# Performance work log

Hardware: AMD Instinct MI355X
Metric: run time of the kernel (lower is better)

## Reference

```python
import jax, jax.numpy as jnp
import numpy as np

N = 50000      # nodes
E = 800000     # edges
D_IN = 300     # input node feature dim
D_H = 96       # hidden dim
D_OUT = 2      # classes
G = 64         # graphs in batch


def setup_inputs() -> dict:
    key = jax.random.key(0)
    ks = jax.random.split(key, 10)
    x = jax.random.normal(ks[0], (N, D_IN), dtype=jnp.float32)
    src = jax.random.randint(ks[1], (E,), 0, N, dtype=jnp.int32)
    dst = jax.random.randint(ks[2], (E,), 0, N, dtype=jnp.int32)
    batch = jnp.sort(jax.random.randint(ks[3], (N,), 0, G, dtype=jnp.int32))
    # GCNConv: linear weight (no bias in lin), separate additive bias (PyG default)
    W1 = jax.random.normal(ks[4], (D_IN, D_H), jnp.float32) / np.sqrt(D_IN)
    b1 = jnp.zeros((D_H,), jnp.float32)
    W2 = jax.random.normal(ks[5], (D_H, D_H), jnp.float32) / np.sqrt(D_H)
    b2 = jnp.zeros((D_H,), jnp.float32)
    Wfc = jax.random.normal(ks[6], (D_H, D_OUT), jnp.float32) / np.sqrt(D_H)
    bfc = jnp.zeros((D_OUT,), jnp.float32)
    return {"x": x, "W1": W1, "b1": b1, "W2": W2, "b2": b2,
            "Wfc": Wfc, "bfc": bfc, "src": src, "dst": dst, "batch": batch}


def _gcn_conv(h_in, W, b, src, dst, deg_inv_sqrt):
    """PyG GCNConv with self-loops: out = D^-1/2 (A+I) D^-1/2 (h W) + b."""
    h = h_in @ W                                   # [N, F] transform first
    norm = deg_inv_sqrt[src] * deg_inv_sqrt[dst]   # [E]
    msg = h[src] * norm[:, None]                   # gather + scale (dominant traffic)
    agg = jax.ops.segment_sum(msg, dst, num_segments=N)
    agg = agg + h * (deg_inv_sqrt * deg_inv_sqrt)[:, None]  # self-loop term
    return agg + b


def reference(x, W1, b1, W2, b2, Wfc, bfc, src, dst, batch):
    # degree with self loops, computed on destination nodes (PyG convention)
    deg = jax.ops.segment_sum(jnp.ones((E,), x.dtype), dst, num_segments=N) + 1.0
    dis = jax.lax.rsqrt(deg)
    h = jax.nn.relu(_gcn_conv(x, W1, b1, src, dst, dis))   # dropout = identity (eval)
    h = jax.nn.relu(_gcn_conv(h, W2, b2, src, dst, dis))
    # global mean pool over per-graph node segments
    counts = jax.ops.segment_sum(jnp.ones((N,), x.dtype), batch, num_segments=G)
    pooled = jax.ops.segment_sum(h, batch, num_segments=G) / jnp.maximum(counts, 1.0)[:, None]
    return pooled @ Wfc + bfc                               # [G, D_OUT]
```

## Files before the change

kernel.cpp:

```cpp
#include <hip/hip_runtime.h>
#include <hip/hip_bf16.h>

#define NN 50000
#define NE 800000
#define DIN 300
#define KP1 320
#define DH 96
#define DOUTC 2
#define NG 64

#define NKB 10
#define NFRAG (NKB * 6 * 64)

#define DSTRIDE 64

typedef __attribute__((ext_vector_type(8))) short bf16x8;
typedef __attribute__((ext_vector_type(4))) float f32x4;

__device__ inline unsigned short f2bf(float f) {
    unsigned int u = __float_as_uint(f);
    unsigned int r = (u + 0x7fffu + ((u >> 16) & 1u)) >> 16;
    return (unsigned short)r;
}
__device__ inline float b2f(unsigned short u) {
    return __uint_as_float((unsigned int)u << 16);
}

__global__ void k_init(int* cnt, float* pooled, int* gcnt) {
    int i = blockIdx.x * blockDim.x + threadIdx.x;
    if (i < NN) cnt[i] = 0;
    if (i < NG * DH) pooled[i] = 0.f;
    if (i < NG) gcnt[i] = 0;
}

__global__ void k_scatcnt(const int* __restrict__ src, const int* __restrict__ dst,
                          int* cnt, unsigned short* __restrict__ esrc) {
    int e = blockIdx.x * blockDim.x + threadIdx.x;
    if (e < NE) {
        int d = dst[e];
        int pos = atomicAdd(&cnt[d], 1);
        if (pos < DSTRIDE) esrc[(size_t)d * DSTRIDE + pos] = (unsigned short)src[e];
    }
}

__global__ void k_dis(const int* __restrict__ cnt, float* __restrict__ dis) {
    int i = blockIdx.x * blockDim.x + threadIdx.x;
    if (i < NN) dis[i] = rsqrtf(1.0f + (float)cnt[i]);
}

__global__ void k_wt(const float* __restrict__ W, unsigned short* __restrict__ WT,
                     int K, int KPAD) {
    int i = blockIdx.x * blockDim.x + threadIdx.x;
    if (i >= DH * KPAD) return;
    int j = i / KPAD, k = i - j * KPAD;
    WT[i] = (k < K) ? f2bf(W[(size_t)k * DH + j]) : (unsigned short)0;
}

__global__ void k_wt1f(const float* __restrict__ W, unsigned short* __restrict__ WF) {
    int g = blockIdx.x * blockDim.x + threadIdx.x;
    if (g >= NFRAG * 8) return;
    int j = g & 7;
    int f = g >> 3;
    int lane = f & 63;
    int ft = f >> 6;
    int t = ft % 6;
    int i = ft / 6;
    int row = (lane & 15) + 16 * t;
    int col = i * 32 + (lane >> 4) * 8 + j;
    WF[g] = (col < DIN) ? f2bf(W[(size_t)col * DH + row]) : (unsigned short)0;
}

__global__ __launch_bounds__(256) void k_gemm1(const float* __restrict__ A,
        const unsigned short* __restrict__ WF, unsigned short* __restrict__ Cb) {
    __shared__ unsigned short ldsB[NFRAG * 8];
    const int tid = threadIdx.x;
    {
        const uint4* srcv = (const uint4*)WF;
        uint4* dstv = (uint4*)ldsB;
        #pragma unroll
        for (int f = 0; f < NFRAG / 256; ++f)
            dstv[f * 256 + tid] = srcv[f * 256 + tid];
    }
    __syncthreads();

    const int wv = tid >> 6;
    const int lane = tid & 63;
    const int m = lane & 15;
    const int quad = lane >> 4;
    const int row = blockIdx.x * 64 + wv * 16 + m;
    const int arow = row < NN ? row : NN - 1;
    const float* ap = A + (size_t)arow * DIN + quad * 8;
    const float4 z4 = make_float4(0.f, 0.f, 0.f, 0.f);
    const bf16x8* lb = (const bf16x8*)ldsB;
    f32x4 acc[6];
    #pragma unroll
    for (int t = 0; t < 6; ++t) acc[t] = (f32x4){0.f, 0.f, 0.f, 0.f};

    float4 pa[4][2];
    #pragma unroll
    for (int i = 0; i < 3; ++i) {
        int kb = i * 32 + quad * 8;
        pa[i][0] = (kb + 4 <= DIN) ? *(const float4*)(ap + i * 32) : z4;
        pa[i][1] = (kb + 8 <= DIN) ? *(const float4*)(ap + i * 32 + 4) : z4;
    }

    #pragma unroll
    for (int i = 0; i < NKB; ++i) {
        if (i + 3 < NKB) {
            int kb = (i + 3) * 32 + quad * 8;
            pa[(i + 3) & 3][0] = (kb + 4 <= DIN) ? *(const float4*)(ap + (i + 3) * 32) : z4;
            pa[(i + 3) & 3][1] = (kb + 8 <= DIN) ? *(const float4*)(ap + (i + 3) * 32 + 4) : z4;
        }
        float4 a0 = pa[i & 3][0], a1 = pa[i & 3][1];
        bf16x8 af;
        af[0] = (short)f2bf(a0.x); af[1] = (short)f2bf(a0.y);
        af[2] = (short)f2bf(a0.z); af[3] = (short)f2bf(a0.w);
        af[4] = (short)f2bf(a1.x); af[5] = (short)f2bf(a1.y);
        af[6] = (short)f2bf(a1.z); af[7] = (short)f2bf(a1.w);
        #pragma unroll
        for (int t = 0; t < 6; ++t) {
            bf16x8 bf = lb[(i * 6 + t) * 64 + lane];
            acc[t] = __builtin_amdgcn_mfma_f32_16x16x32_bf16(af, bf, acc[t], 0, 0, 0);
        }
    }
    const int rbase = blockIdx.x * 64 + wv * 16 + quad * 4;
    #pragma unroll
    for (int r = 0; r < 4; ++r) {
        int rr = rbase + r;
        if (rr < NN) {
            unsigned short* cp = Cb + (size_t)rr * DH + m;
            #pragma unroll
            for (int t = 0; t < 6; ++t) cp[t * 16] = f2bf(acc[t][r]);
        }
    }
}

__global__ __launch_bounds__(256) void k_gemm2(const unsigned short* __restrict__ Ab,
        const unsigned short* __restrict__ WT, unsigned short* __restrict__ Cb) {
    const int tid = threadIdx.x;
    const int wv = tid >> 6;
    const int lane = tid & 63;
    const int m = lane & 15;
    const int quad = lane >> 4;
    const int row = blockIdx.x * 64 + wv * 16 + m;
    const int arow = row < NN ? row : NN - 1;
    const unsigned short* ap = Ab + (size_t)arow * DH + quad * 8;
    const unsigned short* wp = WT + (size_t)m * DH + quad * 8;
    bf16x8 af[3], bf[3][6];
    #pragma unroll
    for (int i = 0; i < 3; ++i) af[i] = *(const bf16x8*)(ap + i * 32);
    #pragma unroll
    for (int i = 0; i < 3; ++i)
        #pragma unroll
        for (int t = 0; t < 6; ++t)
            bf[i][t] = *(const bf16x8*)(wp + (size_t)t * 16 * DH + i * 32);
    f32x4 acc[6];
    #pragma unroll
    for (int t = 0; t < 6; ++t) acc[t] = (f32x4){0.f, 0.f, 0.f, 0.f};
    #pragma unroll
    for (int i = 0; i < 3; ++i)
        #pragma unroll
        for (int t = 0; t < 6; ++t)
            acc[t] = __builtin_amdgcn_mfma_f32_16x16x32_bf16(af[i], bf[i][t], acc[t], 0, 0, 0);
    const int rbase = blockIdx.x * 64 + wv * 16 + quad * 4;
    #pragma unroll
    for (int r = 0; r < 4; ++r) {
        int rr = rbase + r;
        if (rr < NN) {
            unsigned short* cp = Cb + (size_t)rr * DH + m;
            #pragma unroll
            for (int t = 0; t < 6; ++t) cp[t * 16] = f2bf(acc[t][r]);
        }
    }
}

#define QH (DH / 4)
template <bool BFOUT>
__global__ void k_agg(const ushort4* __restrict__ hb, const float* __restrict__ dis,
                      const int* __restrict__ cnt,
                      const unsigned short* __restrict__ esrc,
                      const float4* __restrict__ bias4, float4* __restrict__ fout,
                      ushort4* __restrict__ bout) {
    int gid = blockIdx.x * blockDim.x + threadIdx.x;
    if (gid >= NN * QH) return;
    int n = gid / QH;
    int q = gid - n * QH;
    int count = cnt[n];
    if (count > DSTRIDE) count = DSTRIDE;
    const int beg = n * DSTRIDE;
    const int end = beg + count;
    float dn = dis[n];
    ushort4 u0 = hb[(size_t)n * QH + q];
    float4 acc = make_float4(dn * b2f(u0.x), dn * b2f(u0.y), dn * b2f(u0.z), dn * b2f(u0.w));
    int e = beg;
    for (; e + 3 < end; e += 4) {
        int s0 = esrc[e], s1 = esrc[e + 1], s2 = esrc[e + 2], s3 = esrc[e + 3];
        float d0 = dis[s0], d1 = dis[s1], d2 = dis[s2], d3 = dis[s3];
        ushort4 v0 = hb[(size_t)s0 * QH + q];
        ushort4 v1 = hb[(size_t)s1 * QH + q];
        ushort4 v2 = hb[(size_t)s2 * QH + q];
        ushort4 v3 = hb[(size_t)s3 * QH + q];
        acc.x = fmaf(d0, b2f(v0.x), acc.x); acc.y = fmaf(d0, b2f(v0.y), acc.y);
        acc.z = fmaf(d0, b2f(v0.z), acc.z); acc.w = fmaf(d0, b2f(v0.w), acc.w);
        acc.x = fmaf(d1, b2f(v1.x), acc.x); acc.y = fmaf(d1, b2f(v1.y), acc.y);
        acc.z = fmaf(d1, b2f(v1.z), acc.z); acc.w = fmaf(d1, b2f(v1.w), acc.w);
        acc.x = fmaf(d2, b2f(v2.x), acc.x); acc.y = fmaf(d2, b2f(v2.y), acc.y);
        acc.z = fmaf(d2, b2f(v2.z), acc.z); acc.w = fmaf(d2, b2f(v2.w), acc.w);
        acc.x = fmaf(d3, b2f(v3.x), acc.x); acc.y = fmaf(d3, b2f(v3.y), acc.y);
        acc.z = fmaf(d3, b2f(v3.z), acc.z); acc.w = fmaf(d3, b2f(v3.w), acc.w);
    }
    for (; e < end; ++e) {
        int s = esrc[e];
        float ds = dis[s];
        ushort4 v = hb[(size_t)s * QH + q];
        acc.x = fmaf(ds, b2f(v.x), acc.x);
        acc.y = fmaf(ds, b2f(v.y), acc.y);
        acc.z = fmaf(ds, b2f(v.z), acc.z);
        acc.w = fmaf(ds, b2f(v.w), acc.w);
    }
    float4 b = bias4[q];
    float4 r;
    r.x = fmaxf(fmaf(dn, acc.x, b.x), 0.f);
    r.y = fmaxf(fmaf(dn, acc.y, b.y), 0.f);
    r.z = fmaxf(fmaf(dn, acc.z, b.z), 0.f);
    r.w = fmaxf(fmaf(dn, acc.w, b.w), 0.f);
    if (BFOUT) {
        ushort4 o;
        o.x = f2bf(r.x); o.y = f2bf(r.y); o.z = f2bf(r.z); o.w = f2bf(r.w);
        bout[gid] = o;
    } else {
        fout[gid] = r;
    }
}

#define PNODES 32
__global__ void k_pool_partial(const float* __restrict__ h, const int* __restrict__ batch,
                               float* __restrict__ pooled, int* __restrict__ gcnt) {
    __shared__ int sbatch[PNODES];
    const int n0 = blockIdx.x * PNODES;
    const int nend = min(n0 + PNODES, NN);
    const int cnt = nend - n0;
    const int f = threadIdx.x;
    if (f < cnt) sbatch[f] = batch[n0 + f];
    __syncthreads();
    if (f < DH) {
        float acc = 0.f;
        int cur = sbatch[0];
        for (int i = 0; i < cnt; ++i) {
            int g = sbatch[i];
            if (g != cur) {
                atomicAdd(&pooled[cur * DH + f], acc);
                acc = 0.f; cur = g;
            }
            acc += h[(size_t)(n0 + i) * DH + f];
        }
        atomicAdd(&pooled[cur * DH + f], acc);
    } else if (f == DH) {
        int c = 0;
        int cur = sbatch[0];
        for (int i = 0; i < cnt; ++i) {
            int g = sbatch[i];
            if (g != cur) { atomicAdd(&gcnt[cur], c); c = 0; cur = g; }
            ++c;
        }
        atomicAdd(&gcnt[cur], c);
    }
}

__global__ void k_fc(const float* __restrict__ pooled, const int* __restrict__ gcnt,
                     const float* __restrict__ Wfc, const float* __restrict__ bfc,
                     float* __restrict__ out) {
    const int t = threadIdx.x;
    if (t >= NG * DOUTC) return;
    const int g = t / DOUTC;
    const int c = t - g * DOUTC;
    float inv = 1.f / fmaxf((float)gcnt[g], 1.f);
    float acc = bfc[c];
    #pragma unroll 8
    for (int j = 0; j < DH; ++j)
        acc += pooled[g * DH + j] * inv * Wfc[j * DOUTC + c];
    out[g * DOUTC + c] = acc;
}

extern "C" void kernel_launch(void* const* d_in, const int* in_sizes, int n_in,
                              void* d_out, int out_size, void* d_ws, size_t ws_size,
                              hipStream_t stream) {
    const float* x   = (const float*)d_in[0];
    const float* W1  = (const float*)d_in[1];
    const float* b1  = (const float*)d_in[2];
    const float* W2  = (const float*)d_in[3];
    const float* b2  = (const float*)d_in[4];
    const float* Wfc = (const float*)d_in[5];
    const float* bfc = (const float*)d_in[6];
    const int* src   = (const int*)d_in[7];
    const int* dst   = (const int*)d_in[8];
    const int* batch = (const int*)d_in[9];
    float* out = (float*)d_out;

    unsigned short* hb  = (unsigned short*)d_ws;
    unsigned short* a1b = hb + (size_t)NN * DH;
    float* hbuf  = (float*)(a1b + (size_t)NN * DH);
    float* dis   = hbuf + (size_t)NN * DH;
    float* pooled= dis + NN;
    int* cnt     = (int*)(pooled + NG * DH);
    int* gcnt    = cnt + NN;
    unsigned short* esrc = (unsigned short*)(gcnt + NG);
    unsigned short* wt1f = esrc + (size_t)NN * DSTRIDE;
    unsigned short* wt2  = wt1f + NFRAG * 8;

    const int TB = 256;
    k_init<<<(NN + TB - 1) / TB, TB, 0, stream>>>(cnt, pooled, gcnt);
    k_scatcnt<<<(NE + TB - 1) / TB, TB, 0, stream>>>(src, dst, cnt, esrc);
    k_dis<<<(NN + TB - 1) / TB, TB, 0, stream>>>(cnt, dis);
    k_wt1f<<<(NFRAG * 8 + TB - 1) / TB, TB, 0, stream>>>(W1, wt1f);
    k_wt<<<(DH * DH + TB - 1) / TB, TB, 0, stream>>>(W2, wt2, DH, DH);

    k_gemm1<<<(NN + 63) / 64, 256, 0, stream>>>(x, wt1f, hb);
    k_agg<true><<<(NN * QH + TB - 1) / TB, TB, 0, stream>>>(
        (const ushort4*)hb, dis, cnt, esrc, (const float4*)b1,
        nullptr, (ushort4*)a1b);
    k_gemm2<<<(NN + 63) / 64, 256, 0, stream>>>(a1b, wt2, hb);
    k_agg<false><<<(NN * QH + TB - 1) / TB, TB, 0, stream>>>(
        (const ushort4*)hb, dis, cnt, esrc, (const float4*)b2,
        (float4*)hbuf, nullptr);
    k_pool_partial<<<(NN + PNODES - 1) / PNODES, 128, 0, stream>>>(hbuf, batch, pooled, gcnt);
    k_fc<<<1, 128, 0, stream>>>(pooled, gcnt, Wfc, bfc, out);
}
```

Before: 262.0 us.

## Fuse edge scatter into GEMM1, pooling into second aggregation, merge prep kernels

Merges init and weight-layout kernels into one prep kernel and moves the edge-bucketing scatter into the tail of the first GEMM kernel. The second aggregation now atomically accumulates its ReLU output directly into per-graph pooled sums, removing the fp32 hidden buffer and the separate pooling kernel. Graph node counts are recovered by binary search over the sorted batch array in the final FC kernel. This cuts launches and a large write/read, but adds heavily contended float atomics on a small pooled array.

```diff
diff --git a/kernel.cpp b/kernel.cpp
--- a/kernel.cpp
+++ b/kernel.cpp
@@ -13,6 +13,8 @@
 #define NFRAG (NKB * 6 * 64)
 
 #define DSTRIDE 64
+#define NB1 ((NN + 63) / 64)
+#define EPB 1024
 
 typedef __attribute__((ext_vector_type(8))) short bf16x8;
 typedef __attribute__((ext_vector_type(4))) float f32x4;
@@ -26,20 +28,26 @@
     return __uint_as_float((unsigned int)u << 16);
 }
 
-__global__ void k_init(int* cnt, float* pooled, int* gcnt) {
+__global__ void k_prep(int* cnt, float* pooled,
+                       const float* __restrict__ W1, unsigned short* __restrict__ wt1f,
+                       const float* __restrict__ W2, unsigned short* __restrict__ wt2) {
     int i = blockIdx.x * blockDim.x + threadIdx.x;
     if (i < NN) cnt[i] = 0;
     if (i < NG * DH) pooled[i] = 0.f;
-    if (i < NG) gcnt[i] = 0;
-}
-
-__global__ void k_scatcnt(const int* __restrict__ src, const int* __restrict__ dst,
-                          int* cnt, unsigned short* __restrict__ esrc) {
-    int e = blockIdx.x * blockDim.x + threadIdx.x;
-    if (e < NE) {
-        int d = dst[e];
-        int pos = atomicAdd(&cnt[d], 1);
-        if (pos < DSTRIDE) esrc[(size_t)d * DSTRIDE + pos] = (unsigned short)src[e];
+    if (i < NFRAG * 8) {
+        int j = i & 7;
+        int f = i >> 3;
+        int lane = f & 63;
+        int ft = f >> 6;
+        int t = ft % 6;
+        int kb = ft / 6;
+        int row = (lane & 15) + 16 * t;
+        int col = kb * 32 + (lane >> 4) * 8 + j;
+        wt1f[i] = (col < DIN) ? f2bf(W1[(size_t)col * DH + row]) : (unsigned short)0;
+    }
+    if (i < DH * DH) {
+        int j = i / DH, k = i - j * DH;
+        wt2[i] = f2bf(W2[(size_t)k * DH + j]);
     }
 }
 
@@ -48,30 +56,10 @@
     if (i < NN) dis[i] = rsqrtf(1.0f + (float)cnt[i]);
 }
 
-__global__ void k_wt(const float* __restrict__ W, unsigned short* __restrict__ WT,
-                     int K, int KPAD) {
-    int i = blockIdx.x * blockDim.x + threadIdx.x;
-    if (i >= DH * KPAD) return;
-    int j = i / KPAD, k = i - j * KPAD;
-    WT[i] = (k < K) ? f2bf(W[(size_t)k * DH + j]) : (unsigned short)0;
-}
-
-__global__ void k_wt1f(const float* __restrict__ W, unsigned short* __restrict__ WF) {
-    int g = blockIdx.x * blockDim.x + threadIdx.x;
-    if (g >= NFRAG * 8) return;
-    int j = g & 7;
-    int f = g >> 3;
-    int lane = f & 63;
-    int ft = f >> 6;
-    int t = ft % 6;
-    int i = ft / 6;
-    int row = (lane & 15) + 16 * t;
-    int col = i * 32 + (lane >> 4) * 8 + j;
-    WF[g] = (col < DIN) ? f2bf(W[(size_t)col * DH + row]) : (unsigned short)0;
-}
-
-__global__ __launch_bounds__(256) void k_gemm1(const float* __restrict__ A,
-        const unsigned short* __restrict__ WF, unsigned short* __restrict__ Cb) {
+__global__ __launch_bounds__(256) void k_gemm1s(const float* __restrict__ A,
+        const unsigned short* __restrict__ WF, unsigned short* __restrict__ Cb,
+        const int* __restrict__ src, const int* __restrict__ dst,
+        int* cnt, unsigned short* __restrict__ esrc) {
     __shared__ unsigned short ldsB[NFRAG * 8];
     const int tid = threadIdx.x;
     {
@@ -131,6 +119,17 @@
             unsigned short* cp = Cb + (size_t)rr * DH + m;
             #pragma unroll
             for (int t = 0; t < 6; ++t) cp[t * 16] = f2bf(acc[t][r]);
+        }
+    }
+
+    const int ebase = blockIdx.x * EPB;
+    #pragma unroll
+    for (int k = 0; k < EPB / 256; ++k) {
+        int e = ebase + k * 256 + tid;
+        if (e < NE) {
+            int d = dst[e];
+            int pos = atomicAdd(&cnt[d], 1);
+            if (pos < DSTRIDE) esrc[(size_t)d * DSTRIDE + pos] = (unsigned short)src[e];
         }
     }
 }
@@ -179,7 +178,8 @@
 __global__ void k_agg(const ushort4* __restrict__ hb, const float* __restrict__ dis,
                       const int* __restrict__ cnt,
                       const unsigned short* __restrict__ esrc,
-                      const float4* __restrict__ bias4, float4* __restrict__ fout,
+                      const float4* __restrict__ bias4,
+                      const int* __restrict__ batch, float* __restrict__ pooled,
                       ushort4* __restrict__ bout) {
     int gid = blockIdx.x * blockDim.x + threadIdx.x;
     if (gid >= NN * QH) return;
@@ -229,52 +229,27 @@
         o.x = f2bf(r.x); o.y = f2bf(r.y); o.z = f2bf(r.z); o.w = f2bf(r.w);
         bout[gid] = o;
     } else {
-        fout[gid] = r;
-    }
-}
-
-#define PNODES 32
-__global__ void k_pool_partial(const float* __restrict__ h, const int* __restrict__ batch,
-                               float* __restrict__ pooled, int* __restrict__ gcnt) {
-    __shared__ int sbatch[PNODES];
-    const int n0 = blockIdx.x * PNODES;
-    const int nend = min(n0 + PNODES, NN);
-    const int cnt = nend - n0;
-    const int f = threadIdx.x;
-    if (f < cnt) sbatch[f] = batch[n0 + f];
-    __syncthreads();
-    if (f < DH) {
-        float acc = 0.f;
-        int cur = sbatch[0];
-        for (int i = 0; i < cnt; ++i) {
-            int g = sbatch[i];
-            if (g != cur) {
-                atomicAdd(&pooled[cur * DH + f], acc);
-                acc = 0.f; cur = g;
-            }
-            acc += h[(size_t)(n0 + i) * DH + f];
-        }
-        atomicAdd(&pooled[cur * DH + f], acc);
-    } else if (f == DH) {
-        int c = 0;
-        int cur = sbatch[0];
-        for (int i = 0; i < cnt; ++i) {
-            int g = sbatch[i];
-            if (g != cur) { atomicAdd(&gcnt[cur], c); c = 0; cur = g; }
-            ++c;
-        }
-        atomicAdd(&gcnt[cur], c);
-    }
-}
-
-__global__ void k_fc(const float* __restrict__ pooled, const int* __restrict__ gcnt,
+        float* pp = &pooled[batch[n] * DH + q * 4];
+        atomicAdd(pp + 0, r.x);
+        atomicAdd(pp + 1, r.y);
+        atomicAdd(pp + 2, r.z);
+        atomicAdd(pp + 3, r.w);
+    }
+}
+
+__global__ void k_fc(const float* __restrict__ pooled, const int* __restrict__ batch,
                      const float* __restrict__ Wfc, const float* __restrict__ bfc,
                      float* __restrict__ out) {
     const int t = threadIdx.x;
     if (t >= NG * DOUTC) return;
     const int g = t / DOUTC;
     const int c = t - g * DOUTC;
-    float inv = 1.f / fmaxf((float)gcnt[g], 1.f);
+    int lo = 0, hi = NN;
+    while (lo < hi) { int mid = (lo + hi) >> 1; if (batch[mid] < g) lo = mid + 1; else hi = mid; }
+    const int s = lo;
+    hi = NN;
+    while (lo < hi) { int mid = (lo + hi) >> 1; if (batch[mid] < g + 1) lo = mid + 1; else hi = mid; }
+    float inv = 1.f / fmaxf((float)(lo - s), 1.f);
     float acc = bfc[c];
     #pragma unroll 8
     for (int j = 0; j < DH; ++j)
@@ -299,30 +274,23 @@
 
     unsigned short* hb  = (unsigned short*)d_ws;
     unsigned short* a1b = hb + (size_t)NN * DH;
-    float* hbuf  = (float*)(a1b + (size_t)NN * DH);
-    float* dis   = hbuf + (size_t)NN * DH;
+    float* dis   = (float*)(a1b + (size_t)NN * DH);
     float* pooled= dis + NN;
     int* cnt     = (int*)(pooled + NG * DH);
-    int* gcnt    = cnt + NN;
-    unsigned short* esrc = (unsigned short*)(gcnt + NG);
+    unsigned short* esrc = (unsigned short*)(cnt + NN);
     unsigned short* wt1f = esrc + (size_t)NN * DSTRIDE;
     unsigned short* wt2  = wt1f + NFRAG * 8;
 
     const int TB = 256;
-    k_init<<<(NN + TB - 1) / TB, TB, 0, stream>>>(cnt, pooled, gcnt);
-    k_scatcnt<<<(NE + TB - 1) / TB, TB, 0, stream>>>(src, dst, cnt, esrc);
+    k_prep<<<(NN + TB - 1) / TB, TB, 0, stream>>>(cnt, pooled, W1, wt1f, W2, wt2);
+    k_gemm1s<<<NB1, 256, 0, stream>>>(x, wt1f, hb, src, dst, cnt, esrc);
     k_dis<<<(NN + TB - 1) / TB, TB, 0, stream>>>(cnt, dis);
-    k_wt1f<<<(NFRAG * 8 + TB - 1) / TB, TB, 0, stream>>>(W1, wt1f);
-    k_wt<<<(DH * DH + TB - 1) / TB, TB, 0, stream>>>(W2, wt2, DH, DH);
-
-    k_gemm1<<<(NN + 63) / 64, 256, 0, stream>>>(x, wt1f, hb);
     k_agg<true><<<(NN * QH + TB - 1) / TB, TB, 0, stream>>>(
         (const ushort4*)hb, dis, cnt, esrc, (const float4*)b1,
-        nullptr, (ushort4*)a1b);
-    k_gemm2<<<(NN + 63) / 64, 256, 0, stream>>>(a1b, wt2, hb);
+        nullptr, nullptr, (ushort4*)a1b);
+    k_gemm2<<<NB1, 256, 0, stream>>>(a1b, wt2, hb);
     k_agg<false><<<(NN * QH + TB - 1) / TB, TB, 0, stream>>>(
         (const ushort4*)hb, dis, cnt, esrc, (const float4*)b2,
-        (float4*)hbuf, nullptr);
-    k_pool_partial<<<(NN + PNODES - 1) / PNODES, 128, 0, stream>>>(hbuf, batch, pooled, gcnt);
-    k_fc<<<1, 128, 0, stream>>>(pooled, gcnt, Wfc, bfc, out);
-}
+        batch, pooled, nullptr);
+    k_fc<<<1, 128, 0, stream>>>(pooled, batch, Wfc, bfc, out);
+}
```

New measurement: 454.2 us. +73.3%, slower.
